# Kernel optimization log

Measured on AMD Instinct MI355X. Metric: run time of the kernel, lower is better.

The kernel has to match this reference:

```python
import jax, jax.numpy as jnp
import numpy as np

N = 50000
E = 800000
IN_DIM = 768
HID = 128
OUT = 128
R = 8


def rgcn_conv(x, edge_index, edge_type, weight, root, bias, num_relations):
    # PyG RGCNConv (aggr='mean'): per-relation transform of source nodes,
    # mean-aggregated at destination per relation, plus root transform + bias.
    n = x.shape[0]
    src, dst = edge_index[0], edge_index[1]
    # [R, N, out]: transform every node by every relation weight (R is small)
    h_all = jnp.einsum('ni,rio->rno', x, weight)
    msg = h_all[edge_type, src]  # [E, out] gathered per-edge message
    # per-(dst, relation) mean normalization
    seg = dst * num_relations + edge_type
    counts = jax.ops.segment_sum(jnp.ones((src.shape[0],), dtype=x.dtype), seg,
                                 num_segments=n * num_relations)
    norm = 1.0 / jnp.maximum(counts[seg], 1.0)
    agg = jax.ops.segment_sum(msg * norm[:, None], dst, num_segments=n)
    return agg + x @ root + bias


def setup_inputs() -> dict:
    key = jax.random.key(0)
    ks = jax.random.split(key, 9)
    feature = jax.random.normal(ks[0], (N, IN_DIM), dtype=jnp.float32)
    edge_index = jax.random.randint(ks[1], (2, E), 0, N, dtype=jnp.int64 if jax.config.jax_enable_x64 else jnp.int32)
    edge_type = jax.random.randint(ks[2], (E,), 0, R, dtype=edge_index.dtype)
    s1 = 1.0 / np.sqrt(IN_DIM)
    s2 = 1.0 / np.sqrt(HID)
    w1 = jax.random.uniform(ks[3], (R, IN_DIM, HID), jnp.float32, -s1, s1)
    root1 = jax.random.uniform(ks[4], (IN_DIM, HID), jnp.float32, -s1, s1)
    b1 = jnp.zeros((HID,), jnp.float32)
    w2 = jax.random.uniform(ks[5], (R, HID, OUT), jnp.float32, -s2, s2)
    root2 = jax.random.uniform(ks[6], (HID, OUT), jnp.float32, -s2, s2)
    b2 = jnp.zeros((OUT,), jnp.float32)
    return {"feature": feature, "edge_index": edge_index, "edge_type": edge_type,
            "w1": w1, "root1": root1, "b1": b1, "w2": w2, "root2": root2, "b2": b2}


def reference(feature, edge_index, edge_type, w1, root1, b1, w2, root2, b2):
    x = rgcn_conv(feature, edge_index, edge_type, w1, root1, b1, R)
    x = jax.nn.relu(x)
    # dropout(p=0.5) is identity in eval mode
    x = rgcn_conv(x, edge_index, edge_type, w2, root2, b2, R)
    return jnp.concatenate((feature, x), axis=1)
```

## Files before the change

kernel.cpp:

```cpp
#include <hip/hip_runtime.h>
#include <hip/hip_bf16.h>


typedef __hip_bfloat16 bf16;
typedef __attribute__((ext_vector_type(4))) float f32x4;
typedef __attribute__((ext_vector_type(8))) short s16x8;

#define IN_DIM 768
#define NREL   8

__device__ __forceinline__ void gload16(const void* g, void* l) {
    __builtin_amdgcn_global_load_lds(
        (const __attribute__((address_space(1))) void*)g,
        (__attribute__((address_space(3))) void*)l, 16, 0, 0);
}

template <bool RELU, bool AGGBIAS, bool GUARD, typename OutT>
__global__ __launch_bounds__(256) void mfma_gemm(
    const bf16* __restrict__ A, int lda,
    const bf16* __restrict__ BT, long brel,
    const float* __restrict__ agg, const float* __restrict__ bias,
    OutT* __restrict__ C, long crel, int ldc, int coff,
    int M, int K, int nmt, int swz_nrel)
{
    __shared__ bf16 Asm[128 * 64];
    __shared__ bf16 Bsm[128 * 64];

    const int tid  = threadIdx.x;
    const int lane = tid & 63;
    const int wrow = ((tid >> 7) & 1) * 64;
    const int wcol = ((tid >> 6) & 1) * 64;

    int mtile, rel;
    if (swz_nrel == 0) {
        mtile = blockIdx.x; rel = 0;
    } else {
        const int id  = blockIdx.x;
        const int tot = nmt * swz_nrel;
        const int per = tot >> 3;
        const int w   = (id & 7) * per + (id >> 3);
        rel   = w % swz_nrel;
        mtile = w / swz_nrel;
    }
    const long m0 = (long)mtile * 128;
    const bf16* Bp = BT + (long)rel * brel;

    f32x4 acc[4][4];
#pragma unroll
    for (int i = 0; i < 4; ++i)
#pragma unroll
        for (int j = 0; j < 4; ++j) acc[i][j] = (f32x4){0.f, 0.f, 0.f, 0.f};

    for (int k0 = 0; k0 < K; k0 += 64) {
#pragma unroll
        for (int i = 0; i < 4; ++i) {
            const int flat = i * 256 + tid;
            const int row  = flat >> 3;
            const int sch  = (flat & 7) ^ (row & 7);
            char* ldsA = (char*)Asm + (i * 256 + (tid & 192)) * 16;
            char* ldsB = (char*)Bsm + (i * 256 + (tid & 192)) * 16;
            gload16(A  + (m0 + row) * (long)lda + k0 + sch * 8, ldsA);
            gload16(Bp + (long)row * K          + k0 + sch * 8, ldsB);
        }
        __syncthreads();

#pragma unroll
        for (int ks = 0; ks < 2; ++ks) {
            s16x8 af[4], bfr[4];
            const int g = ks * 4 + (lane >> 4);
#pragma unroll
            for (int i = 0; i < 4; ++i) {
                const int ar = wrow + i * 16 + (lane & 15);
                af[i] = *(const s16x8*)((const char*)Asm + ar * 128 +
                                        (g ^ (ar & 7)) * 16);
                const int br = wcol + i * 16 + (lane & 15);
                bfr[i] = *(const s16x8*)((const char*)Bsm + br * 128 +
                                         (g ^ (br & 7)) * 16);
            }
#pragma unroll
            for (int i = 0; i < 4; ++i)
#pragma unroll
                for (int j = 0; j < 4; ++j)
                    acc[i][j] = __builtin_amdgcn_mfma_f32_16x16x32_bf16(
                        af[i], bfr[j], acc[i][j], 0, 0, 0);
        }
        __syncthreads();
    }

    float breg[4];
    if (AGGBIAS) {
#pragma unroll
        for (int j = 0; j < 4; ++j) breg[j] = bias[wcol + j * 16 + (lane & 15)];
    }
    OutT* Cp = C + (long)rel * crel;
#pragma unroll
    for (int i = 0; i < 4; ++i) {
#pragma unroll
        for (int r = 0; r < 4; ++r) {
            const long row = m0 + wrow + i * 16 + (lane >> 4) * 4 + r;
            if (GUARD && row >= M) continue;
#pragma unroll
            for (int j = 0; j < 4; ++j) {
                float v = acc[i][j][r];
                const int col = wcol + j * 16 + (lane & 15);
                if (AGGBIAS) v += agg[row * 128 + col] + breg[j];
                if (RELU) v = fmaxf(v, 0.f);
                if constexpr (sizeof(OutT) == 2)
                    Cp[row * (long)ldc + coff + col] = __float2bfloat16(v);
                else
                    Cp[row * (long)ldc + coff + col] = v;
            }
        }
    }
}

__global__ __launch_bounds__(256) void rgcn_count(
    const int* __restrict__ edst, const int* __restrict__ etype, int E,
    float* __restrict__ counts)
{
    const int e = blockIdx.x * blockDim.x + threadIdx.x;
    if (e < E) atomicAdd(&counts[(long)edst[e] * NREL + etype[e]], 1.0f);
}

__global__ __launch_bounds__(256) void deg_block_scan(
    const float* __restrict__ counts, int N, int* __restrict__ rowstart,
    int* __restrict__ partials)
{
    __shared__ int s[256];
    const int d = blockIdx.x * 256 + threadIdx.x;
    int deg = 0;
    if (d < N) {
#pragma unroll
        for (int t = 0; t < NREL; ++t) deg += (int)counts[(long)d * NREL + t];
    }
    s[threadIdx.x] = deg;
    __syncthreads();
    for (int off = 1; off < 256; off <<= 1) {
        int v = (threadIdx.x >= off) ? s[threadIdx.x - off] : 0;
        __syncthreads();
        s[threadIdx.x] += v;
        __syncthreads();
    }
    if (d < N) rowstart[d] = s[threadIdx.x] - deg;
    if (threadIdx.x == 255) partials[blockIdx.x] = s[255];
}

__global__ __launch_bounds__(256) void scan_partials(int* partials, int nb)
{
    __shared__ int s[256];
    const int v = (threadIdx.x < nb) ? partials[threadIdx.x] : 0;
    s[threadIdx.x] = v;
    __syncthreads();
    for (int off = 1; off < 256; off <<= 1) {
        int u = (threadIdx.x >= off) ? s[threadIdx.x - off] : 0;
        __syncthreads();
        s[threadIdx.x] += u;
        __syncthreads();
    }
    if (threadIdx.x < nb) partials[threadIdx.x] = s[threadIdx.x] - v;
}

__global__ __launch_bounds__(256) void add_base(
    int* __restrict__ rowstart, const int* __restrict__ partials, int N, int E)
{
    const int d = blockIdx.x * 256 + threadIdx.x;
    if (d < N) rowstart[d] += partials[blockIdx.x];
    if (d == 0) rowstart[N] = E;
}

__global__ __launch_bounds__(256) void csr_fill(
    const int* __restrict__ esrc, const int* __restrict__ edst,
    const int* __restrict__ etype, int E, const int* __restrict__ rowstart,
    int* __restrict__ cursor, int* __restrict__ epack)
{
    const int e = blockIdx.x * 256 + threadIdx.x;
    if (e >= E) return;
    const int d = edst[e];
    const int pos = atomicAdd(&cursor[d], 1);
    epack[rowstart[d] + pos] = esrc[e] | (etype[e] << 24);
}

__global__ __launch_bounds__(256) void rgcn_gather(
    const int* __restrict__ rowstart, const int* __restrict__ epack,
    const float* __restrict__ counts, const bf16* __restrict__ h, long hrel,
    float* __restrict__ agg, int N, int NP)
{
    const int wid  = (blockIdx.x * 256 + threadIdx.x) >> 6;
    const int lane = threadIdx.x & 63;
    if (wid >= NP) return;
    float accx = 0.f, accy = 0.f;
    if (wid < N) {
        const int start = rowstart[wid];
        const int end   = rowstart[wid + 1];
        const float nrm =
            1.0f / fmaxf(counts[(long)wid * NREL + (lane & 7)], 1.0f);
        for (int base = start; base < end; base += 64) {
            const int rem = end - base;
            const int cnt = rem < 64 ? rem : 64;
            int w = 0;
            if (lane < rem) w = epack[base + lane];
            for (int i = 0; i < cnt; ++i) {
                const int word = __shfl(w, i);
                const int src  = word & 0xFFFFFF;
                const int t    = ((unsigned)word) >> 24;
                const float norm = __shfl(nrm, t);
                const ushort2 raw = *(const ushort2*)(
                    h + (long)t * hrel + (long)src * 128 + (lane << 1));
                accx += __uint_as_float((unsigned)raw.x << 16) * norm;
                accy += __uint_as_float((unsigned)raw.y << 16) * norm;
            }
        }
    }
    *(float2*)(agg + (long)wid * 128 + (lane << 1)) =
        make_float2(accx, accy);
}

__global__ __launch_bounds__(256) void rgcn_scatter(
    const int* __restrict__ esrc, const int* __restrict__ edst,
    const int* __restrict__ etype, int E, int filter, long hrel,
    const float* __restrict__ counts, const bf16* __restrict__ h,
    float* __restrict__ agg)
{
    const long gt = (long)blockIdx.x * 256 + threadIdx.x;
    const int  w  = (int)(gt >> 6);
    if (w >= E) return;
    const int t = etype[w];
    if (filter >= 0 && t != filter) return;
    const int lane = threadIdx.x & 63;
    const int s = esrc[w], d = edst[w];
    const float norm = 1.0f / fmaxf(counts[(long)d * NREL + t], 1.0f);
    const bf16* hp = h + (filter >= 0 ? 0L : (long)t * hrel) +
                     (long)s * 128 + (lane << 1);
    const ushort2 raw = *(const ushort2*)hp;
    float* ap = agg + (long)d * 128 + (lane << 1);
    atomicAdd(ap,     __uint_as_float((unsigned)raw.x << 16) * norm);
    atomicAdd(ap + 1, __uint_as_float((unsigned)raw.y << 16) * norm);
}

__global__ __launch_bounds__(256) void cvt_f32_bf16(
    const float* __restrict__ x, bf16* __restrict__ y, long n8)
{
    const long i = (long)blockIdx.x * 256 + threadIdx.x;
    if (i >= n8) return;
    const float4 a = *(const float4*)(x + i * 8);
    const float4 b = *(const float4*)(x + i * 8 + 4);
    bf16 o[8];
    o[0] = __float2bfloat16(a.x); o[1] = __float2bfloat16(a.y);
    o[2] = __float2bfloat16(a.z); o[3] = __float2bfloat16(a.w);
    o[4] = __float2bfloat16(b.x); o[5] = __float2bfloat16(b.y);
    o[6] = __float2bfloat16(b.z); o[7] = __float2bfloat16(b.w);
    *(s16x8*)(y + i * 8) = *(const s16x8*)o;
}

__global__ __launch_bounds__(256) void cvt_w_transpose(
    const float* __restrict__ w, bf16* __restrict__ wt, int K, long total)
{
    const long idx = (long)blockIdx.x * 256 + threadIdx.x;
    if (idx >= total) return;
    const int  k  = (int)(idx % K);
    const long rn = idx / K;
    const int  n  = (int)(rn & 127);
    const long r  = rn >> 7;
    wt[idx] = __float2bfloat16(w[(r * K + k) * 128 + n]);
}

__global__ __launch_bounds__(256) void rgcn_copy_feat(
    const float* __restrict__ f, float* __restrict__ out, int N)
{
    const int idx   = blockIdx.x * blockDim.x + threadIdx.x;
    const int total = N * (IN_DIM / 4);
    if (idx >= total) return;
    const int n  = idx / (IN_DIM / 4);
    const int k4 = (idx % (IN_DIM / 4)) << 2;
    *(float4*)&out[(long)n * (IN_DIM + 128) + k4] =
        *(const float4*)&f[(long)n * IN_DIM + k4];
}

extern "C" void kernel_launch(void* const* d_in, const int* in_sizes, int n_in,
                              void* d_out, int out_size, void* d_ws,
                              size_t ws_size, hipStream_t stream)
{
    const float* feature = (const float*)d_in[0];
    const int*   eidx    = (const int*)d_in[1];
    const int*   etype   = (const int*)d_in[2];
    const float* w1      = (const float*)d_in[3];
    const float* root1   = (const float*)d_in[4];
    const float* b1      = (const float*)d_in[5];
    const float* w2      = (const float*)d_in[6];
    const float* root2   = (const float*)d_in[7];
    const float* b2      = (const float*)d_in[8];

    const int N = in_sizes[0] / IN_DIM;
    const int E = in_sizes[2];
    const int* esrc = eidx;
    const int* edst = eidx + E;
    const int NMT = (N + 127) / 128;
    const int NP  = NMT * 128;

    char* p = (char*)d_ws;
    auto carve = [&](size_t b) { char* q = p; p += (b + 255) & ~(size_t)255; return q; };
    float* counts   = (float*)carve((size_t)N * NREL * 4);
    float* agg      = (float*)carve((size_t)NP * 128 * 4);
    bf16*  x1b      = (bf16*)carve((size_t)NP * 128 * 2);
    bf16*  fb       = (bf16*)carve((size_t)NP * IN_DIM * 2);
    bf16*  w1T      = (bf16*)carve((size_t)NREL * 128 * IN_DIM * 2);
    bf16*  w2T      = (bf16*)carve((size_t)NREL * 128 * 128 * 2);
    bf16*  r1T      = (bf16*)carve((size_t)128 * IN_DIM * 2);
    bf16*  r2T      = (bf16*)carve((size_t)128 * 128 * 2);
    int*   rowstart = (int*)carve((size_t)(N + 1) * 4);
    int*   cursor   = (int*)carve((size_t)N * 4);
    int*   partials = (int*)carve(1024);
    int*   epack    = (int*)carve((size_t)E * 4);
    const size_t used_base = (size_t)(p - (char*)d_ws);
    const size_t h_full    = (size_t)NREL * NP * 128 * 2;
    const bool   full      = ws_size >= used_base + h_full;
    bf16* h = (bf16*)carve(full ? h_full : (size_t)NP * 128 * 2);
    const long hrel = (long)NP * 128;

    const int count_blks = (E + 255) / 256;
    const int copy_blks  = (N * (IN_DIM / 4) + 255) / 256;
    const int nblk       = (N + 255) / 256;
    const int gat_blks   = (NP * 64) / 256;
    const int scat_blks  = (int)(((long)E * 64 + 255) / 256);

    {
        const long n8 = (long)N * IN_DIM / 8;
        cvt_f32_bf16<<<(int)((n8 + 255) / 256), 256, 0, stream>>>(feature, fb, n8);
        long t1 = (long)NREL * 128 * IN_DIM;
        cvt_w_transpose<<<(int)((t1 + 255) / 256), 256, 0, stream>>>(w1, w1T, IN_DIM, t1);
        long t2 = (long)NREL * 128 * 128;
        cvt_w_transpose<<<(int)((t2 + 255) / 256), 256, 0, stream>>>(w2, w2T, 128, t2);
        long t3 = (long)128 * IN_DIM;
        cvt_w_transpose<<<(int)((t3 + 255) / 256), 256, 0, stream>>>(root1, r1T, IN_DIM, t3);
        long t4 = (long)128 * 128;
        cvt_w_transpose<<<(int)((t4 + 255) / 256), 256, 0, stream>>>(root2, r2T, 128, t4);
    }

    hipMemsetAsync(counts, 0, (size_t)N * NREL * 4, stream);
    rgcn_count<<<count_blks, 256, 0, stream>>>(edst, etype, E, counts);
    if (full) {
        deg_block_scan<<<nblk, 256, 0, stream>>>(counts, N, rowstart, partials);
        scan_partials<<<1, 256, 0, stream>>>(partials, nblk);
        add_base<<<nblk, 256, 0, stream>>>(rowstart, partials, N, E);
        hipMemsetAsync(cursor, 0, (size_t)N * 4, stream);
        csr_fill<<<count_blks, 256, 0, stream>>>(esrc, edst, etype, E,
                                                 rowstart, cursor, epack);
    }

    if (full) {
        mfma_gemm<false, false, false, bf16><<<NMT * NREL, 256, 0, stream>>>(
            fb, IN_DIM, w1T, (long)128 * IN_DIM, nullptr, nullptr,
            h, hrel, 128, 0, N, IN_DIM, NMT, NREL);
        rgcn_gather<<<gat_blks, 256, 0, stream>>>(
            rowstart, epack, counts, h, hrel, agg, N, NP);
    } else {
        hipMemsetAsync(agg, 0, (size_t)NP * 128 * 4, stream);
        for (int r = 0; r < NREL; ++r) {
            mfma_gemm<false, false, false, bf16><<<NMT, 256, 0, stream>>>(
                fb, IN_DIM, w1T + (long)r * 128 * IN_DIM, 0, nullptr, nullptr,
                h, 0, 128, 0, N, IN_DIM, NMT, 0);
            rgcn_scatter<<<scat_blks, 256, 0, stream>>>(
                esrc, edst, etype, E, r, 0, counts, h, agg);
        }
    }
    mfma_gemm<true, true, false, bf16><<<NMT, 256, 0, stream>>>(
        fb, IN_DIM, r1T, 0, agg, b1, x1b, 0, 128, 0, N, IN_DIM, NMT, 0);

    if (full) {
        mfma_gemm<false, false, false, bf16><<<NMT * NREL, 256, 0, stream>>>(
            x1b, 128, w2T, (long)128 * 128, nullptr, nullptr,
            h, hrel, 128, 0, N, 128, NMT, NREL);
        rgcn_gather<<<gat_blks, 256, 0, stream>>>(
            rowstart, epack, counts, h, hrel, agg, N, NP);
    } else {
        hipMemsetAsync(agg, 0, (size_t)NP * 128 * 4, stream);
        for (int r = 0; r < NREL; ++r) {
            mfma_gemm<false, false, false, bf16><<<NMT, 256, 0, stream>>>(
                x1b, 128, w2T + (long)r * 128 * 128, 0, nullptr, nullptr,
                h, 0, 128, 0, N, 128, NMT, 0);
            rgcn_scatter<<<scat_blks, 256, 0, stream>>>(
                esrc, edst, etype, E, r, 0, counts, h, agg);
        }
    }
    mfma_gemm<false, true, true, float><<<NMT, 256, 0, stream>>>(
        x1b, 128, r2T, 0, agg, b2, (float*)d_out, 0, IN_DIM + 128, IN_DIM,
        N, 128, NMT, 0);
    rgcn_copy_feat<<<copy_blks, 256, 0, stream>>>(feature, (float*)d_out, N);
}
```

Measured before the change: 506.2 us.

## Fuse root transform into relation GEMM with node-major h layout and bf16 agg

```diff
diff --git a/kernel.cpp b/kernel.cpp
--- a/kernel.cpp
+++ b/kernel.cpp
@@ -8,6 +8,16 @@
 
 #define IN_DIM 768
 #define NREL   8
+#define NTL    9
+#define LDH    (NTL*128)
+
+__device__ __forceinline__ float bf2f(unsigned short u) {
+    return __uint_as_float((unsigned)u << 16);
+}
+__device__ __forceinline__ unsigned short f2bf(float f) {
+    __hip_bfloat16 b = __float2bfloat16(f);
+    return *(unsigned short*)&b;
+}
 
 __device__ __forceinline__ void gload16(const void* g, void* l) {
     __builtin_amdgcn_global_load_lds(
@@ -15,13 +25,9 @@
         (__attribute__((address_space(3))) void*)l, 16, 0, 0);
 }
 
-template <bool RELU, bool AGGBIAS, bool GUARD, typename OutT>
 __global__ __launch_bounds__(256) void mfma_gemm(
-    const bf16* __restrict__ A, int lda,
-    const bf16* __restrict__ BT, long brel,
-    const float* __restrict__ agg, const float* __restrict__ bias,
-    OutT* __restrict__ C, long crel, int ldc, int coff,
-    int M, int K, int nmt, int swz_nrel)
+    const bf16* __restrict__ A, int lda, const bf16* __restrict__ BT,
+    bf16* __restrict__ C, int K, int nmt, int ntl)
 {
     __shared__ bf16 Asm[128 * 64];
     __shared__ bf16 Bsm[128 * 64];
@@ -31,19 +37,18 @@
     const int wrow = ((tid >> 7) & 1) * 64;
     const int wcol = ((tid >> 6) & 1) * 64;
 
-    int mtile, rel;
-    if (swz_nrel == 0) {
-        mtile = blockIdx.x; rel = 0;
-    } else {
-        const int id  = blockIdx.x;
-        const int tot = nmt * swz_nrel;
-        const int per = tot >> 3;
-        const int w   = (id & 7) * per + (id >> 3);
-        rel   = w % swz_nrel;
-        mtile = w / swz_nrel;
-    }
-    const long m0 = (long)mtile * 128;
-    const bf16* Bp = BT + (long)rel * brel;
+    const int nwg  = nmt * ntl;
+    const int orig = blockIdx.x;
+    const int xcd  = orig & 7;
+    const int q    = nwg >> 3, rr = nwg & 7;
+    const int bse  = (xcd < rr) ? xcd * (q + 1) : rr * (q + 1) + (xcd - rr) * q;
+    const int w    = bse + (orig >> 3);
+    const int ntile = w % ntl;
+    const int mtile = w / ntl;
+    const long m0   = (long)mtile * 128;
+    const bf16* Bp  = BT + (long)ntile * 128 * K;
+    const int  ldh  = ntl * 128;
+    const int  ncol0 = ntile * 128;
 
     f32x4 acc[4][4];
 #pragma unroll
@@ -87,28 +92,16 @@
         __syncthreads();
     }
 
-    float breg[4];
-    if (AGGBIAS) {
-#pragma unroll
-        for (int j = 0; j < 4; ++j) breg[j] = bias[wcol + j * 16 + (lane & 15)];
-    }
-    OutT* Cp = C + (long)rel * crel;
 #pragma unroll
     for (int i = 0; i < 4; ++i) {
 #pragma unroll
         for (int r = 0; r < 4; ++r) {
             const long row = m0 + wrow + i * 16 + (lane >> 4) * 4 + r;
-            if (GUARD && row >= M) continue;
 #pragma unroll
             for (int j = 0; j < 4; ++j) {
-                float v = acc[i][j][r];
                 const int col = wcol + j * 16 + (lane & 15);
-                if (AGGBIAS) v += agg[row * 128 + col] + breg[j];
-                if (RELU) v = fmaxf(v, 0.f);
-                if constexpr (sizeof(OutT) == 2)
-                    Cp[row * (long)ldc + coff + col] = __float2bfloat16(v);
-                else
-                    Cp[row * (long)ldc + coff + col] = v;
+                C[row * (long)ldh + ncol0 + col] =
+                    __float2bfloat16(acc[i][j][r]);
             }
         }
     }
@@ -182,13 +175,15 @@
 
 __global__ __launch_bounds__(256) void rgcn_gather(
     const int* __restrict__ rowstart, const int* __restrict__ epack,
-    const float* __restrict__ counts, const bf16* __restrict__ h, long hrel,
-    float* __restrict__ agg, int N, int NP)
+    const float* __restrict__ counts, const bf16* __restrict__ h,
+    bf16* __restrict__ agg, int N, int NP)
 {
     const int wid  = (blockIdx.x * 256 + threadIdx.x) >> 6;
+    if (wid >= NP) return;
     const int lane = threadIdx.x & 63;
-    if (wid >= NP) return;
-    float accx = 0.f, accy = 0.f;
+    const int half = lane >> 5;
+    const int l32  = lane & 31;
+    float a0 = 0.f, a1 = 0.f, a2 = 0.f, a3 = 0.f;
     if (wid < N) {
         const int start = rowstart[wid];
         const int end   = rowstart[wid + 1];
@@ -197,59 +192,101 @@
         for (int base = start; base < end; base += 64) {
             const int rem = end - base;
             const int cnt = rem < 64 ? rem : 64;
-            int w = 0;
-            if (lane < rem) w = epack[base + lane];
-            for (int i = 0; i < cnt; ++i) {
-                const int word = __shfl(w, i);
-                const int src  = word & 0xFFFFFF;
-                const int t    = ((unsigned)word) >> 24;
+            int wv = 0;
+            if (lane < cnt) wv = epack[base + lane];
+            for (int i = 0; i < cnt; i += 2) {
+                const int  idx   = i + half;
+                const bool valid = idx < cnt;
+                const int  word  = __shfl(wv, idx);
+                int src = 0, t = 0;
+                if (valid) { src = word & 0xFFFFFF; t = ((unsigned)word) >> 24; }
                 const float norm = __shfl(nrm, t);
-                const ushort2 raw = *(const ushort2*)(
-                    h + (long)t * hrel + (long)src * 128 + (lane << 1));
-                accx += __uint_as_float((unsigned)raw.x << 16) * norm;
-                accy += __uint_as_float((unsigned)raw.y << 16) * norm;
+                if (valid) {
+                    const ushort4 raw = *(const ushort4*)(
+                        h + (long)src * LDH + t * 128 + l32 * 4);
+                    a0 += bf2f(raw.x) * norm;
+                    a1 += bf2f(raw.y) * norm;
+                    a2 += bf2f(raw.z) * norm;
+                    a3 += bf2f(raw.w) * norm;
+                }
             }
         }
     }
-    *(float2*)(agg + (long)wid * 128 + (lane << 1)) =
-        make_float2(accx, accy);
-}
-
-__global__ __launch_bounds__(256) void rgcn_scatter(
-    const int* __restrict__ esrc, const int* __restrict__ edst,
-    const int* __restrict__ etype, int E, int filter, long hrel,
-    const float* __restrict__ counts, const bf16* __restrict__ h,
-    float* __restrict__ agg)
-{
-    const long gt = (long)blockIdx.x * 256 + threadIdx.x;
-    const int  w  = (int)(gt >> 6);
-    if (w >= E) return;
-    const int t = etype[w];
-    if (filter >= 0 && t != filter) return;
-    const int lane = threadIdx.x & 63;
-    const int s = esrc[w], d = edst[w];
-    const float norm = 1.0f / fmaxf(counts[(long)d * NREL + t], 1.0f);
-    const bf16* hp = h + (filter >= 0 ? 0L : (long)t * hrel) +
-                     (long)s * 128 + (lane << 1);
-    const ushort2 raw = *(const ushort2*)hp;
-    float* ap = agg + (long)d * 128 + (lane << 1);
-    atomicAdd(ap,     __uint_as_float((unsigned)raw.x << 16) * norm);
-    atomicAdd(ap + 1, __uint_as_float((unsigned)raw.y << 16) * norm);
-}
-
-__global__ __launch_bounds__(256) void cvt_f32_bf16(
-    const float* __restrict__ x, bf16* __restrict__ y, long n8)
-{
-    const long i = (long)blockIdx.x * 256 + threadIdx.x;
-    if (i >= n8) return;
-    const float4 a = *(const float4*)(x + i * 8);
-    const float4 b = *(const float4*)(x + i * 8 + 4);
+    a0 += __shfl(a0, lane ^ 32);
+    a1 += __shfl(a1, lane ^ 32);
+    a2 += __shfl(a2, lane ^ 32);
+    a3 += __shfl(a3, lane ^ 32);
+    if (half == 0) {
+        ushort4 o;
+        o.x = f2bf(a0); o.y = f2bf(a1); o.z = f2bf(a2); o.w = f2bf(a3);
+        *(ushort4*)(agg + (long)wid * 128 + l32 * 4) = o;
+    }
+}
+
+__global__ __launch_bounds__(256) void epilogue1(
+    const bf16* __restrict__ h, const bf16* __restrict__ agg,
+    const float* __restrict__ b1, bf16* __restrict__ x1b, int NP)
+{
+    const int idx = blockIdx.x * 256 + threadIdx.x;
+    if (idx >= NP * 16) return;
+    const int n  = idx >> 4;
+    const int c8 = (idx & 15) << 3;
+    const s16x8 hv = *(const s16x8*)(h + (long)n * LDH + NREL * 128 + c8);
+    const s16x8 av = *(const s16x8*)(agg + (long)n * 128 + c8);
+    const float4 bA = *(const float4*)(b1 + c8);
+    const float4 bB = *(const float4*)(b1 + c8 + 4);
+    const float bb[8] = {bA.x, bA.y, bA.z, bA.w, bB.x, bB.y, bB.z, bB.w};
+    bf16 o[8];
+#pragma unroll
+    for (int j = 0; j < 8; ++j) {
+        float v = bf2f((unsigned short)hv[j]) +
+                  bf2f((unsigned short)av[j]) + bb[j];
+        o[j] = __float2bfloat16(fmaxf(v, 0.f));
+    }
+    *(s16x8*)(x1b + (long)n * 128 + c8) = *(const s16x8*)o;
+}
+
+__global__ __launch_bounds__(256) void epilogue2(
+    const bf16* __restrict__ h, const bf16* __restrict__ agg,
+    const float* __restrict__ b2, float* __restrict__ out, int N)
+{
+    const int idx = blockIdx.x * 256 + threadIdx.x;
+    if (idx >= N * 16) return;
+    const int n  = idx >> 4;
+    const int c8 = (idx & 15) << 3;
+    const s16x8 hv = *(const s16x8*)(h + (long)n * LDH + NREL * 128 + c8);
+    const s16x8 av = *(const s16x8*)(agg + (long)n * 128 + c8);
+    const float4 bA = *(const float4*)(b2 + c8);
+    const float4 bB = *(const float4*)(b2 + c8 + 4);
+    const float bb[8] = {bA.x, bA.y, bA.z, bA.w, bB.x, bB.y, bB.z, bB.w};
+    float v[8];
+#pragma unroll
+    for (int j = 0; j < 8; ++j)
+        v[j] = bf2f((unsigned short)hv[j]) + bf2f((unsigned short)av[j]) + bb[j];
+    float* op = out + (long)n * (IN_DIM + 128) + IN_DIM + c8;
+    *(float4*)op       = make_float4(v[0], v[1], v[2], v[3]);
+    *(float4*)(op + 4) = make_float4(v[4], v[5], v[6], v[7]);
+}
+
+__global__ __launch_bounds__(256) void cvt_copy(
+    const float* __restrict__ f, bf16* __restrict__ fb,
+    float* __restrict__ out, int N)
+{
+    const int idx = blockIdx.x * 256 + threadIdx.x;
+    if (idx >= N * (IN_DIM / 8)) return;
+    const int n  = idx / (IN_DIM / 8);
+    const int k8 = (idx % (IN_DIM / 8)) << 3;
+    const float4 a = *(const float4*)(f + (long)n * IN_DIM + k8);
+    const float4 b = *(const float4*)(f + (long)n * IN_DIM + k8 + 4);
+    float* op = out + (long)n * (IN_DIM + 128) + k8;
+    *(float4*)op       = a;
+    *(float4*)(op + 4) = b;
     bf16 o[8];
     o[0] = __float2bfloat16(a.x); o[1] = __float2bfloat16(a.y);
     o[2] = __float2bfloat16(a.z); o[3] = __float2bfloat16(a.w);
     o[4] = __float2bfloat16(b.x); o[5] = __float2bfloat16(b.y);
     o[6] = __float2bfloat16(b.z); o[7] = __float2bfloat16(b.w);
-    *(s16x8*)(y + i * 8) = *(const s16x8*)o;
+    *(s16x8*)(fb + (long)n * IN_DIM + k8) = *(const s16x8*)o;
 }
 
 __global__ __launch_bounds__(256) void cvt_w_transpose(
@@ -262,18 +299,6 @@
     const int  n  = (int)(rn & 127);
     const long r  = rn >> 7;
     wt[idx] = __float2bfloat16(w[(r * K + k) * 128 + n]);
-}
-
-__global__ __launch_bounds__(256) void rgcn_copy_feat(
-    const float* __restrict__ f, float* __restrict__ out, int N)
-{
-    const int idx   = blockIdx.x * blockDim.x + threadIdx.x;
-    const int total = N * (IN_DIM / 4);
-    if (idx >= total) return;
-    const int n  = idx / (IN_DIM / 4);
-    const int k4 = (idx % (IN_DIM / 4)) << 2;
-    *(float4*)&out[(long)n * (IN_DIM + 128) + k4] =
-        *(const float4*)&f[(long)n * IN_DIM + k4];
 }
 
 extern "C" void kernel_launch(void* const* d_in, const int* in_sizes, int n_in,
@@ -300,90 +325,59 @@
     char* p = (char*)d_ws;
     auto carve = [&](size_t b) { char* q = p; p += (b + 255) & ~(size_t)255; return q; };
     float* counts   = (float*)carve((size_t)N * NREL * 4);
-    float* agg      = (float*)carve((size_t)NP * 128 * 4);
+    bf16*  agg      = (bf16*)carve((size_t)NP * 128 * 2);
     bf16*  x1b      = (bf16*)carve((size_t)NP * 128 * 2);
     bf16*  fb       = (bf16*)carve((size_t)NP * IN_DIM * 2);
-    bf16*  w1T      = (bf16*)carve((size_t)NREL * 128 * IN_DIM * 2);
-    bf16*  w2T      = (bf16*)carve((size_t)NREL * 128 * 128 * 2);
-    bf16*  r1T      = (bf16*)carve((size_t)128 * IN_DIM * 2);
-    bf16*  r2T      = (bf16*)carve((size_t)128 * 128 * 2);
+    bf16*  w1m      = (bf16*)carve((size_t)NTL * 128 * IN_DIM * 2);
+    bf16*  w2m      = (bf16*)carve((size_t)NTL * 128 * 128 * 2);
     int*   rowstart = (int*)carve((size_t)(N + 1) * 4);
     int*   cursor   = (int*)carve((size_t)N * 4);
     int*   partials = (int*)carve(1024);
     int*   epack    = (int*)carve((size_t)E * 4);
-    const size_t used_base = (size_t)(p - (char*)d_ws);
-    const size_t h_full    = (size_t)NREL * NP * 128 * 2;
-    const bool   full      = ws_size >= used_base + h_full;
-    bf16* h = (bf16*)carve(full ? h_full : (size_t)NP * 128 * 2);
-    const long hrel = (long)NP * 128;
+    bf16*  h        = (bf16*)carve((size_t)NP * LDH * 2);
+    (void)ws_size;
 
     const int count_blks = (E + 255) / 256;
-    const int copy_blks  = (N * (IN_DIM / 4) + 255) / 256;
     const int nblk       = (N + 255) / 256;
-    const int gat_blks   = (NP * 64) / 256;
-    const int scat_blks  = (int)(((long)E * 64 + 255) / 256);
-
+    const int gat_blks   = NP / 4;
+    const int gemm_blks  = NMT * NTL;
+
+    cvt_copy<<<(N * (IN_DIM / 8) + 255) / 256, 256, 0, stream>>>(
+        feature, fb, (float*)d_out, N);
     {
-        const long n8 = (long)N * IN_DIM / 8;
-        cvt_f32_bf16<<<(int)((n8 + 255) / 256), 256, 0, stream>>>(feature, fb, n8);
         long t1 = (long)NREL * 128 * IN_DIM;
-        cvt_w_transpose<<<(int)((t1 + 255) / 256), 256, 0, stream>>>(w1, w1T, IN_DIM, t1);
+        cvt_w_transpose<<<(int)((t1 + 255) / 256), 256, 0, stream>>>(
+            w1, w1m, IN_DIM, t1);
+        long t1r = (long)128 * IN_DIM;
+        cvt_w_transpose<<<(int)((t1r + 255) / 256), 256, 0, stream>>>(
+            root1, w1m + (long)NREL * 128 * IN_DIM, IN_DIM, t1r);
         long t2 = (long)NREL * 128 * 128;
-        cvt_w_transpose<<<(int)((t2 + 255) / 256), 256, 0, stream>>>(w2, w2T, 128, t2);
-        long t3 = (long)128 * IN_DIM;
-        cvt_w_transpose<<<(int)((t3 + 255) / 256), 256, 0, stream>>>(root1, r1T, IN_DIM, t3);
-        long t4 = (long)128 * 128;
-        cvt_w_transpose<<<(int)((t4 + 255) / 256), 256, 0, stream>>>(root2, r2T, 128, t4);
+        cvt_w_transpose<<<(int)((t2 + 255) / 256), 256, 0, stream>>>(
+            w2, w2m, 128, t2);
+        long t2r = (long)128 * 128;
+        cvt_w_transpose<<<(int)((t2r + 255) / 256), 256, 0, stream>>>(
+            root2, w2m + (long)NREL * 128 * 128, 128, t2r);
     }
 
     hipMemsetAsync(counts, 0, (size_t)N * NREL * 4, stream);
     rgcn_count<<<count_blks, 256, 0, stream>>>(edst, etype, E, counts);
-    if (full) {
-        deg_block_scan<<<nblk, 256, 0, stream>>>(counts, N, rowstart, partials);
-        scan_partials<<<1, 256, 0, stream>>>(partials, nblk);
-        add_base<<<nblk, 256, 0, stream>>>(rowstart, partials, N, E);
-        hipMemsetAsync(cursor, 0, (size_t)N * 4, stream);
-        csr_fill<<<count_blks, 256, 0, stream>>>(esrc, edst, etype, E,
-                                                 rowstart, cursor, epack);
-    }
-
-    if (full) {
-        mfma_gemm<false, false, false, bf16><<<NMT * NREL, 256, 0, stream>>>(
-            fb, IN_DIM, w1T, (long)128 * IN_DIM, nullptr, nullptr,
-            h, hrel, 128, 0, N, IN_DIM, NMT, NREL);
-        rgcn_gather<<<gat_blks, 256, 0, stream>>>(
-            rowstart, epack, counts, h, hrel, agg, N, NP);
-    } else {
-        hipMemsetAsync(agg, 0, (size_t)NP * 128 * 4, stream);
-        for (int r = 0; r < NREL; ++r) {
-            mfma_gemm<false, false, false, bf16><<<NMT, 256, 0, stream>>>(
-                fb, IN_DIM, w1T + (long)r * 128 * IN_DIM, 0, nullptr, nullptr,
-                h, 0, 128, 0, N, IN_DIM, NMT, 0);
-            rgcn_scatter<<<scat_blks, 256, 0, stream>>>(
-                esrc, edst, etype, E, r, 0, counts, h, agg);
-        }
-    }
-    mfma_gemm<true, true, false, bf16><<<NMT, 256, 0, stream>>>(
-        fb, IN_DIM, r1T, 0, agg, b1, x1b, 0, 128, 0, N, IN_DIM, NMT, 0);
-
-    if (full) {
-        mfma_gemm<false, false, false, bf16><<<NMT * NREL, 256, 0, stream>>>(
-            x1b, 128, w2T, (long)128 * 128, nullptr, nullptr,
-            h, hrel, 128, 0, N, 128, NMT, NREL);
-        rgcn_gather<<<gat_blks, 256, 0, stream>>>(
-            rowstart, epack, counts, h, hrel, agg, N, NP);
-    } else {
-        hipMemsetAsync(agg, 0, (size_t)NP * 128 * 4, stream);
-        for (int r = 0; r < NREL; ++r) {
-            mfma_gemm<false, false, false, bf16><<<NMT, 256, 0, stream>>>(
-                x1b, 128, w2T + (long)r * 128 * 128, 0, nullptr, nullptr,
-                h, 0, 128, 0, N, 128, NMT, 0);
-            rgcn_scatter<<<scat_blks, 256, 0, stream>>>(
-                esrc, edst, etype, E, r, 0, counts, h, agg);
-        }
-    }
-    mfma_gemm<false, true, true, float><<<NMT, 256, 0, stream>>>(
-        x1b, 128, r2T, 0, agg, b2, (float*)d_out, 0, IN_DIM + 128, IN_DIM,
-        N, 128, NMT, 0);
-    rgcn_copy_feat<<<copy_blks, 256, 0, stream>>>(feature, (float*)d_out, N);
-}
+    deg_block_scan<<<nblk, 256, 0, stream>>>(counts, N, rowstart, partials);
+    scan_partials<<<1, 256, 0, stream>>>(partials, nblk);
+    add_base<<<nblk, 256, 0, stream>>>(rowstart, partials, N, E);
+    hipMemsetAsync(cursor, 0, (size_t)N * 4, stream);
+    csr_fill<<<count_blks, 256, 0, stream>>>(esrc, edst, etype, E,
+                                             rowstart, cursor, epack);
+
+    mfma_gemm<<<gemm_blks, 256, 0, stream>>>(fb, IN_DIM, w1m, h,
+                                             IN_DIM, NMT, NTL);
+    rgcn_gather<<<gat_blks, 256, 0, stream>>>(rowstart, epack, counts, h,
+                                              agg, N, NP);
+    epilogue1<<<NP / 16, 256, 0, stream>>>(h, agg, b1, x1b, NP);
+
+    mfma_gemm<<<gemm_blks, 256, 0, stream>>>(x1b, 128, w2m, h,
+                                             128, NMT, NTL);
+    rgcn_gather<<<gat_blks, 256, 0, stream>>>(rowstart, epack, counts, h,
+                                              agg, N, NP);
+    epilogue2<<<(N * 16 + 255) / 256, 256, 0, stream>>>(h, agg, b2,
+                                                        (float*)d_out, N);
+}
```

After: 436.9 us. 1.16x faster.
